# Kernel optimization log

Measured on AMD Instinct MI355X. Metric: run time of the kernel, lower is better.

## Reference

```python
import jax, jax.numpy as jnp
import numpy as np


def setup_inputs() -> dict:
    key = jax.random.key(0)
    k1, k2 = jax.random.split(key)
    B, C = 4096, 128
    mu = jax.random.normal(k1, (B, C), dtype=jnp.float32)
    # symmetrize-ish random sigma (any [B,C,C] works; math does not require SPD)
    sigma = jax.random.normal(k2, (B, C, C), dtype=jnp.float32)
    return {"mu": mu, "sigma": sigma}


def reference(mu, sigma):
    # softmax over class dim (dim=1)
    p = jax.nn.softmax(mu, axis=1)                     # [B, C]
    # Jacobian of softmax: J[b,i,j] = p_i * delta_ij - p_i * p_j
    eye = jnp.eye(p.shape[1], dtype=p.dtype)
    J = p[:, :, None] * eye[None] - p[:, :, None] * p[:, None, :]  # [B, C, C]
    # sigma_y = J @ sigma @ J^T
    sigma_y = jnp.einsum('bij,bjk,blk->bil', J, sigma, J)
    return (p, sigma_y)
```

## Files before the change

kernel.cpp:

```cpp
#include <hip/hip_runtime.h>
#include <math.h>


#define C_DIM   128
#define TPB     1024
#define F4_PB   4096
#define KIT     4

typedef float f4 __attribute__((ext_vector_type(4)));

__global__ __launch_bounds__(TPB, 8) void vdp_softmax_kernel(
    const float* __restrict__ mu,
    const float* __restrict__ sigma,
    float* __restrict__ out_p,
    float* __restrict__ out_sy)
{
    const int b    = blockIdx.x;
    const int t    = threadIdx.x;
    const int lane = t & 63;
    const int wave = t >> 6;
    const int colg = t & 31;
    const int rowg = t >> 5;

    __shared__ float lds_p[C_DIM];
    __shared__ float lds_c[C_DIM];
    __shared__ float lds_r[C_DIM];
    __shared__ float lds_rpart[16][C_DIM];
    __shared__ float lds_red[4];

    const f4* sig4 = (const f4*)sigma + (size_t)b * F4_PB;
    f4 v[KIT];
#pragma unroll
    for (int k = 0; k < KIT; ++k)
        v[k] = __builtin_nontemporal_load(&sig4[t + TPB * k]);

    float x = 0.f, e = 0.f;
    if (wave < 2) {
        x = mu[(size_t)b * C_DIM + t];
        float m = x;
#pragma unroll
        for (int off = 32; off >= 1; off >>= 1)
            m = fmaxf(m, __shfl_xor(m, off, 64));
        if (lane == 0) lds_red[wave] = m;
    }
    __syncthreads();
    if (wave < 2) {
        const float gmax = fmaxf(lds_red[0], lds_red[1]);
        e = expf(x - gmax);
        float ssum = e;
#pragma unroll
        for (int off = 32; off >= 1; off >>= 1)
            ssum += __shfl_xor(ssum, off, 64);
        if (lane == 0) lds_red[2 + wave] = ssum;
    }
    __syncthreads();
    if (wave < 2) {
        const float pv = e / (lds_red[2] + lds_red[3]);
        lds_p[t] = pv;
        out_p[(size_t)b * C_DIM + t] = pv;
    }
    __syncthreads();

    const f4 pcol = *(const f4*)&lds_p[4 * colg];

    f4 pr = (f4)(0.f);
    float pc[KIT];
#pragma unroll
    for (int k = 0; k < KIT; ++k) {
        const float prow = lds_p[rowg + 32 * k];
        const f4 vk = v[k];
        pr += prow * vk;
        pc[k] = vk.x * pcol.x + vk.y * pcol.y + vk.z * pcol.z + vk.w * pcol.w;
    }

    pr.x += __shfl_xor(pr.x, 32, 64);
    pr.y += __shfl_xor(pr.y, 32, 64);
    pr.z += __shfl_xor(pr.z, 32, 64);
    pr.w += __shfl_xor(pr.w, 32, 64);
    if (lane < 32)
        *(f4*)&lds_rpart[wave][4 * colg] = pr;

#pragma unroll
    for (int off = 1; off <= 16; off <<= 1) {
#pragma unroll
        for (int k = 0; k < KIT; ++k)
            pc[k] += __shfl_xor(pc[k], off, 64);
    }
    if ((lane & 31) == 0) {
#pragma unroll
        for (int k = 0; k < KIT; ++k)
            lds_c[rowg + 32 * k] = pc[k];
    }
    __syncthreads();

    if (t < C_DIM) {
        float rsum = 0.f;
#pragma unroll
        for (int w = 0; w < 16; ++w)
            rsum += lds_rpart[w][t];
        lds_r[t] = rsum;
    }

    float sval = (t < C_DIM) ? lds_p[t] * lds_c[t] : 0.f;
    if (wave < 2) {
#pragma unroll
        for (int off = 32; off >= 1; off >>= 1)
            sval += __shfl_xor(sval, off, 64);
        if (lane == 0) lds_red[wave] = sval;
    }
    __syncthreads();
    const float s = lds_red[0] + lds_red[1];

    const f4 r4 = *(const f4*)&lds_r[4 * colg];
    f4* out4 = (f4*)out_sy + (size_t)b * F4_PB;
#pragma unroll
    for (int k = 0; k < KIT; ++k) {
        const int row = rowg + 32 * k;
        const float pp   = lds_p[row];
        const float base = s - lds_c[row];
        const f4 vk = v[k];
        f4 o;
        o.x = pp * pcol.x * (vk.x - r4.x + base);
        o.y = pp * pcol.y * (vk.y - r4.y + base);
        o.z = pp * pcol.z * (vk.z - r4.z + base);
        o.w = pp * pcol.w * (vk.w - r4.w + base);
        __builtin_nontemporal_store(o, &out4[t + TPB * k]);
    }
}

extern "C" void kernel_launch(void* const* d_in, const int* in_sizes, int n_in,
                              void* d_out, int out_size, void* d_ws, size_t ws_size,
                              hipStream_t stream) {
    const float* mu    = (const float*)d_in[0];
    const float* sigma = (const float*)d_in[1];
    float* out_p  = (float*)d_out;
    const int B = in_sizes[0] / C_DIM;
    float* out_sy = out_p + (size_t)B * C_DIM;

    vdp_softmax_kernel<<<B, TPB, 0, stream>>>(mu, sigma, out_p, out_sy);
}
```

Baseline: 92.65 us.

## Make kernel persistent over batch groups with register double-buffered sigma prefetch

Each block now processes 16 batches in a loop, prefetching the next batch's sigma tile and mu row into a second register set while the current batch is reduced and written. Softmax is done by a single wave handling two elements per lane, which removes one block barrier per batch. This aims to overlap global loads with reductions and stores and to cut launch and barrier overhead. In exchange, far fewer blocks are launched (one per CU), register pressure rises, and latency hiding now depends on in-block prefetch rather than many resident blocks.

```diff
diff --git a/kernel.cpp b/kernel.cpp
--- a/kernel.cpp
+++ b/kernel.cpp
@@ -2,67 +2,63 @@
 #include <math.h>
 
 
-#define C_DIM   128
-#define TPB     1024
-#define F4_PB   4096
-#define KIT     4
+#define C_DIM 128
+#define TPB   1024
+#define F4_PB 4096
+#define KIT   4
+#define NB    16
 
 typedef float f4 __attribute__((ext_vector_type(4)));
 
-__global__ __launch_bounds__(TPB, 8) void vdp_softmax_kernel(
-    const float* __restrict__ mu,
-    const float* __restrict__ sigma,
-    float* __restrict__ out_p,
-    float* __restrict__ out_sy)
+struct SmemT {
+    float c[C_DIM];
+    float r[C_DIM];
+    float rpart[16][C_DIM];
+    float red;
+};
+
+__device__ __forceinline__ void issue_batch(
+    const f4* __restrict__ sig4, const float* __restrict__ mu,
+    size_t bb, int t, int lane, int wave,
+    f4 (&v)[KIT], float& x0, float& x1)
 {
-    const int b    = blockIdx.x;
-    const int t    = threadIdx.x;
-    const int lane = t & 63;
-    const int wave = t >> 6;
-    const int colg = t & 31;
-    const int rowg = t >> 5;
-
-    __shared__ float lds_p[C_DIM];
-    __shared__ float lds_c[C_DIM];
-    __shared__ float lds_r[C_DIM];
-    __shared__ float lds_rpart[16][C_DIM];
-    __shared__ float lds_red[4];
-
-    const f4* sig4 = (const f4*)sigma + (size_t)b * F4_PB;
-    f4 v[KIT];
+    const f4* s4 = sig4 + bb * F4_PB;
 #pragma unroll
     for (int k = 0; k < KIT; ++k)
-        v[k] = __builtin_nontemporal_load(&sig4[t + TPB * k]);
+        v[k] = __builtin_nontemporal_load(&s4[t + TPB * k]);
+    if (wave == 0) {
+        x0 = mu[bb * C_DIM + lane];
+        x1 = mu[bb * C_DIM + 64 + lane];
+    }
+}
 
-    float x = 0.f, e = 0.f;
-    if (wave < 2) {
-        x = mu[(size_t)b * C_DIM + t];
-        float m = x;
+__device__ __forceinline__ void process_batch(
+    size_t bb, int t, int lane, int wave, int colg, int rowg,
+    f4 (&v)[KIT], float x0, float x1,
+    float* lds_p,
+    SmemT& sm,
+    float* __restrict__ out_p, f4* __restrict__ out_sy)
+{
+    if (wave == 0) {
+        float m = fmaxf(x0, x1);
 #pragma unroll
         for (int off = 32; off >= 1; off >>= 1)
             m = fmaxf(m, __shfl_xor(m, off, 64));
-        if (lane == 0) lds_red[wave] = m;
-    }
-    __syncthreads();
-    if (wave < 2) {
-        const float gmax = fmaxf(lds_red[0], lds_red[1]);
-        e = expf(x - gmax);
-        float ssum = e;
+        const float e0 = expf(x0 - m), e1 = expf(x1 - m);
+        float ss = e0 + e1;
 #pragma unroll
         for (int off = 32; off >= 1; off >>= 1)
-            ssum += __shfl_xor(ssum, off, 64);
-        if (lane == 0) lds_red[2 + wave] = ssum;
-    }
-    __syncthreads();
-    if (wave < 2) {
-        const float pv = e / (lds_red[2] + lds_red[3]);
-        lds_p[t] = pv;
-        out_p[(size_t)b * C_DIM + t] = pv;
+            ss += __shfl_xor(ss, off, 64);
+        const float inv = 1.0f / ss;
+        const float p0 = e0 * inv, p1 = e1 * inv;
+        lds_p[lane] = p0;
+        lds_p[64 + lane] = p1;
+        out_p[bb * C_DIM + lane] = p0;
+        out_p[bb * C_DIM + 64 + lane] = p1;
     }
     __syncthreads();
 
     const f4 pcol = *(const f4*)&lds_p[4 * colg];
-
     f4 pr = (f4)(0.f);
     float pc[KIT];
 #pragma unroll
@@ -72,14 +68,12 @@
         pr += prow * vk;
         pc[k] = vk.x * pcol.x + vk.y * pcol.y + vk.z * pcol.z + vk.w * pcol.w;
     }
-
     pr.x += __shfl_xor(pr.x, 32, 64);
     pr.y += __shfl_xor(pr.y, 32, 64);
     pr.z += __shfl_xor(pr.z, 32, 64);
     pr.w += __shfl_xor(pr.w, 32, 64);
     if (lane < 32)
-        *(f4*)&lds_rpart[wave][4 * colg] = pr;
-
+        *(f4*)&sm.rpart[wave][4 * colg] = pr;
 #pragma unroll
     for (int off = 1; off <= 16; off <<= 1) {
 #pragma unroll
@@ -89,7 +83,7 @@
     if ((lane & 31) == 0) {
 #pragma unroll
         for (int k = 0; k < KIT; ++k)
-            lds_c[rowg + 32 * k] = pc[k];
+            sm.c[rowg + 32 * k] = pc[k];
     }
     __syncthreads();
 
@@ -97,34 +91,69 @@
         float rsum = 0.f;
 #pragma unroll
         for (int w = 0; w < 16; ++w)
-            rsum += lds_rpart[w][t];
-        lds_r[t] = rsum;
+            rsum += sm.rpart[w][t];
+        sm.r[t] = rsum;
     }
-
-    float sval = (t < C_DIM) ? lds_p[t] * lds_c[t] : 0.f;
-    if (wave < 2) {
+    if (wave == 2) {
+        float sv = lds_p[lane] * sm.c[lane] + lds_p[64 + lane] * sm.c[64 + lane];
 #pragma unroll
         for (int off = 32; off >= 1; off >>= 1)
-            sval += __shfl_xor(sval, off, 64);
-        if (lane == 0) lds_red[wave] = sval;
+            sv += __shfl_xor(sv, off, 64);
+        if (lane == 0) sm.red = sv;
     }
     __syncthreads();
-    const float s = lds_red[0] + lds_red[1];
 
-    const f4 r4 = *(const f4*)&lds_r[4 * colg];
-    f4* out4 = (f4*)out_sy + (size_t)b * F4_PB;
+    const f4 r4 = *(const f4*)&sm.r[4 * colg];
+    const float s = sm.red;
+    f4* o4 = out_sy + bb * F4_PB;
 #pragma unroll
     for (int k = 0; k < KIT; ++k) {
         const int row = rowg + 32 * k;
         const float pp   = lds_p[row];
-        const float base = s - lds_c[row];
+        const float base = s - sm.c[row];
         const f4 vk = v[k];
         f4 o;
         o.x = pp * pcol.x * (vk.x - r4.x + base);
         o.y = pp * pcol.y * (vk.y - r4.y + base);
         o.z = pp * pcol.z * (vk.z - r4.z + base);
         o.w = pp * pcol.w * (vk.w - r4.w + base);
-        __builtin_nontemporal_store(o, &out4[t + TPB * k]);
+        __builtin_nontemporal_store(o, &o4[t + TPB * k]);
+    }
+}
+
+__global__ __launch_bounds__(TPB, 4) void vdp_softmax_kernel(
+    const float* __restrict__ mu,
+    const float* __restrict__ sigma,
+    float* __restrict__ out_p,
+    float* __restrict__ out_sy)
+{
+    const int t    = threadIdx.x;
+    const int lane = t & 63;
+    const int wave = t >> 6;
+    const int colg = t & 31;
+    const int rowg = t >> 5;
+
+    __shared__ SmemT sm;
+    __shared__ float lds_p2[2][C_DIM];
+
+    const size_t b0 = (size_t)blockIdx.x * NB;
+    const f4* sig4 = (const f4*)sigma;
+    f4* o4 = (f4*)out_sy;
+
+    f4 vA[KIT], vB[KIT];
+    float xA0 = 0.f, xA1 = 0.f, xB0 = 0.f, xB1 = 0.f;
+
+    issue_batch(sig4, mu, b0, t, lane, wave, vA, xA0, xA1);
+
+#pragma unroll 1
+    for (int it = 0; it < NB; it += 2) {
+        issue_batch(sig4, mu, b0 + it + 1, t, lane, wave, vB, xB0, xB1);
+        process_batch(b0 + it, t, lane, wave, colg, rowg,
+                      vA, xA0, xA1, lds_p2[0], sm, out_p, o4);
+        if (it + 2 < NB)
+            issue_batch(sig4, mu, b0 + it + 2, t, lane, wave, vA, xA0, xA1);
+        process_batch(b0 + it + 1, t, lane, wave, colg, rowg,
+                      vB, xB0, xB1, lds_p2[1], sm, out_p, o4);
     }
 }
 
@@ -137,5 +166,5 @@
     const int B = in_sizes[0] / C_DIM;
     float* out_sy = out_p + (size_t)B * C_DIM;
 
-    vdp_softmax_kernel<<<B, TPB, 0, stream>>>(mu, sigma, out_p, out_sy);
+    vdp_softmax_kernel<<<B / NB, TPB, 0, stream>>>(mu, sigma, out_p, out_sy);
 }
```

Result: slower. 97.89 us (+5.7%).
